# Performance work log

Measured on AMD Instinct MI355X. Metric: run time of the kernel, lower is better.

## Reference

```python
import jax, jax.numpy as jnp
import numpy as np

L, B, T, D, H, M = 2, 4, 1024, 256, 4, 1024
EPS = 1e-5  # hk.LayerNorm default


def setup_inputs() -> dict:
    key = jax.random.key(0)
    ks = jax.random.split(key, 12)
    s_in = (2.0 / D) ** 0.5       # VarianceScaling(2.0), fan_in = D
    s_o = (2.0 / (H * D)) ** 0.5  # fan_in = H*D for final projection
    s_m = (1.0 / M) ** 0.5
    g = lambda k, shape, s: jax.random.normal(k, shape, jnp.float32) * s
    return {
        "queries": g(ks[0], (B, T, D), 1.0),
        "Wq": g(ks[1], (L, D, H * D), s_in),
        "bq": jnp.zeros((L, H * D), jnp.float32),
        "Wk": g(ks[2], (L, D, H * D), s_in),
        "bk": jnp.zeros((L, H * D), jnp.float32),
        "Wv": g(ks[3], (L, D, H * D), s_in),
        "bv": jnp.zeros((L, H * D), jnp.float32),
        "Wo": g(ks[4], (L, H * D, D), s_o),
        "bo": jnp.zeros((L, D), jnp.float32),
        "ln1_s": jnp.ones((L, D), jnp.float32),
        "ln1_b": jnp.zeros((L, D), jnp.float32),
        "W1": g(ks[5], (L, D, M), s_in),
        "b1": jnp.zeros((L, M), jnp.float32),
        "W2": g(ks[6], (L, M, D), s_m),
        "b2": jnp.zeros((L, D), jnp.float32),
        "ln2_s": jnp.ones((L, D), jnp.float32),
        "ln2_b": jnp.zeros((L, D), jnp.float32),
    }


def _layernorm(x, s, o):
    m = jnp.mean(x, axis=-1, keepdims=True)
    v = jnp.var(x, axis=-1, keepdims=True)
    return (x - m) * jax.lax.rsqrt(v + EPS) * s + o


def _block(x, Wq, bq, Wk, bk, Wv, bv, Wo, bo, ln1_s, ln1_b, W1, b1, W2, b2, ln2_s, ln2_b):
    # Multi-head self-attention with per-head dim = D (key_size == qkv_size)
    q = (x @ Wq + bq).reshape(B, T, H, D)
    k = (x @ Wk + bk).reshape(B, T, H, D)
    v = (x @ Wv + bv).reshape(B, T, H, D)
    q = q / jnp.sqrt(jnp.float32(D))
    attn = jnp.einsum('bqhd,bkhd->bhqk', q, k)   # [B,H,T,T]
    attn = jax.nn.softmax(attn, axis=-1)
    o = jnp.einsum('bhqk,bkhd->bqhd', attn, v).reshape(B, T, H * D)
    o = o @ Wo + bo
    # post-norm residual 1
    x = _layernorm(o + x, ln1_s, ln1_b)
    # MLP: Linear(D->M) + ReLU + Linear(M->D)
    h = jax.nn.relu(x @ W1 + b1)
    m = h @ W2 + b2
    return _layernorm(m + x, ln2_s, ln2_b)


def reference(queries, Wq, bq, Wk, bk, Wv, bv, Wo, bo, ln1_s, ln1_b,
              W1, b1, W2, b2, ln2_s, ln2_b):
    x = queries
    for i in range(L):
        x = _block(x, Wq[i], bq[i], Wk[i], bk[i], Wv[i], bv[i], Wo[i], bo[i],
                   ln1_s[i], ln1_b[i], W1[i], b1[i], W2[i], b2[i],
                   ln2_s[i], ln2_b[i])
    return x
```

## Files before the change

### kernel.cpp

```cpp
#include <hip/hip_runtime.h>
#include <hip/hip_bf16.h>

#define CL 2
#define CB 4
#define CT 1024
#define CD 256
#define CH 4
#define CM 1024
#define CHD (CH * CD)
#define NROW (CB * CT)

typedef unsigned short ushort_t;
typedef __attribute__((ext_vector_type(8))) short short8v;
typedef __attribute__((ext_vector_type(4))) float float4v;

#define LOG2E 1.44269504088896f

__device__ __forceinline__ float bf2f(unsigned short u) {
    return __uint_as_float(((unsigned int)u) << 16);
}
__device__ __forceinline__ unsigned short f2bf(float f) {
    unsigned int x = __float_as_uint(f);
    return (unsigned short)((x + 0x7fffu + ((x >> 16) & 1u)) >> 16);
}

__global__ __launch_bounds__(256) void detect_kernel(
    const ushort_t* __restrict__ w, int n, int* __restrict__ flag)
{
    __shared__ int red[256];
    int c = 0;
    for (int i = threadIdx.x; i < n; i += 256) {
        float v = bf2f(w[i]);
        if (!(fabsf(v) <= 1e6f)) c++;
    }
    red[threadIdx.x] = c;
    __syncthreads();
    for (int s = 128; s > 0; s >>= 1) {
        if (threadIdx.x < s) red[threadIdx.x] += red[threadIdx.x + s];
        __syncthreads();
    }
    if (threadIdx.x == 0) flag[0] = (red[0] < 8) ? 1 : 0;
}

__global__ __launch_bounds__(256) void tconv_all(
    const void* __restrict__ Wq, const void* __restrict__ Wk,
    const void* __restrict__ Wv, const void* __restrict__ W1,
    ushort_t* __restrict__ wqkvT, ushort_t* __restrict__ w1T,
    const int* __restrict__ flagp)
{
    const int fbf = *flagp;
    const int z = blockIdx.z;
    const int which = z >> 1, l = z & 1;
    const void* in = (which == 0) ? Wq : (which == 1) ? Wk
                   : (which == 2) ? Wv : W1;
    ushort_t* out = (which < 3)
        ? wqkvT + (long)l * 3072 * 256 + (long)which * 1024 * 256
        : w1T + (long)l * 1024 * 256;
    const long zi = (long)l * 262144;

    __shared__ float tile[32][33];
    const int r0 = blockIdx.y * 32;
    const int c0 = blockIdx.x * 32;
    const int tx = threadIdx.x & 31;
    const int ty = threadIdx.x >> 5;
#pragma unroll
    for (int i = 0; i < 32; i += 8) {
        const long idx = zi + (long)(r0 + ty + i) * 1024 + c0 + tx;
        tile[ty + i][tx] = fbf ? bf2f(((const ushort_t*)in)[idx])
                               : ((const float*)in)[idx];
    }
    __syncthreads();
#pragma unroll
    for (int i = 0; i < 32; i += 8)
        out[(long)(c0 + ty + i) * 256 + r0 + tx] = f2bf(tile[tx][ty + i]);
}

__global__ __launch_bounds__(256) void tconv2(
    const void* __restrict__ Wo, const void* __restrict__ W2,
    ushort_t* __restrict__ wscr, long ioff, const int* __restrict__ flagp)
{
    const int fbf = *flagp;
    const int z = blockIdx.z;
    const void* in = z ? W2 : Wo;
    ushort_t* out = wscr + (long)z * 262144;

    __shared__ float tile[32][33];
    const int r0 = blockIdx.y * 32;
    const int c0 = blockIdx.x * 32;
    const int tx = threadIdx.x & 31;
    const int ty = threadIdx.x >> 5;
#pragma unroll
    for (int i = 0; i < 32; i += 8) {
        const long idx = ioff + (long)(r0 + ty + i) * 256 + c0 + tx;
        tile[ty + i][tx] = fbf ? bf2f(((const ushort_t*)in)[idx])
                               : ((const float*)in)[idx];
    }
    __syncthreads();
#pragma unroll
    for (int i = 0; i < 32; i += 8)
        out[(long)(c0 + ty + i) * 1024 + r0 + tx] = f2bf(tile[tx][ty + i]);
}

__global__ __launch_bounds__(256) void qkv_proj(
    const ushort_t* __restrict__ A, const ushort_t* __restrict__ B,
    const void* __restrict__ bq, const void* __restrict__ bk,
    const void* __restrict__ bv, ushort_t* __restrict__ qk,
    ushort_t* __restrict__ vT, long boff, const int* __restrict__ flagp)
{
    const long m0 = (long)blockIdx.y * 128;
    const long n0 = (long)blockIdx.x * 128;

    __shared__ __align__(16) ushort_t As[128 * 32];
    __shared__ __align__(16) ushort_t Bs[128 * 32];

    const int tid = threadIdx.x;
    const int wave = tid >> 6;
    const int lane = tid & 63;
    const int quad = lane >> 4;
    const int lrow = lane & 15;
    const int wm = (wave >> 1) * 64;
    const int wn = (wave & 1) * 64;

    float4v acc[4][4];
#pragma unroll
    for (int i = 0; i < 4; ++i)
#pragma unroll
        for (int j = 0; j < 4; ++j)
            acc[i][j] = (float4v){0.f, 0.f, 0.f, 0.f};

    for (int k0 = 0; k0 < 256; k0 += 32) {
        __syncthreads();
#pragma unroll
        for (int p = 0; p < 2; ++p) {
            const int c = p * 256 + tid;
            const int row = c >> 2;
            const int kk = (c & 3) << 3;
            *reinterpret_cast<short8v*>(&As[c << 3]) =
                *reinterpret_cast<const short8v*>(&A[(m0 + row) * 256 + k0 + kk]);
            *reinterpret_cast<short8v*>(&Bs[c << 3]) =
                *reinterpret_cast<const short8v*>(&B[(n0 + row) * 256 + k0 + kk]);
        }
        __syncthreads();

        short8v af[4], bfv[4];
#pragma unroll
        for (int i = 0; i < 4; ++i) {
            af[i]  = *reinterpret_cast<const short8v*>(&As[(wm + i * 16 + lrow) * 32 + quad * 8]);
            bfv[i] = *reinterpret_cast<const short8v*>(&Bs[(wn + i * 16 + lrow) * 32 + quad * 8]);
        }
#pragma unroll
        for (int mi = 0; mi < 4; ++mi)
#pragma unroll
            for (int ni = 0; ni < 4; ++ni)
                acc[mi][ni] = __builtin_amdgcn_mfma_f32_16x16x32_bf16(
                    af[mi], bfv[ni], acc[mi][ni], 0, 0, 0);
    }

    const int fbf = *flagp;
#pragma unroll
    for (int mi = 0; mi < 4; ++mi) {
#pragma unroll
        for (int ni = 0; ni < 4; ++ni) {
            const long col = n0 + wn + ni * 16 + lrow;
            const long row0 = m0 + wm + mi * 16 + quad * 4;
            const void* bp;
            long bn;
            if (col < 1024)      { bp = bq; bn = col; }
            else if (col < 2048) { bp = bk; bn = col - 1024; }
            else                 { bp = bv; bn = col - 2048; }
            const float bias = fbf ? bf2f(((const ushort_t*)bp)[boff + bn])
                                   : ((const float*)bp)[boff + bn];
            if (col < 2048) {
#pragma unroll
                for (int r = 0; r < 4; ++r)
                    qk[(row0 + r) * 2048 + col] = f2bf(acc[mi][ni][r] + bias);
            } else {
                const long d = col - 2048;
                const long addr = ((row0 >> 10) << 2) * 262144 + d * 1024 + (row0 & 1023);
                ushort4 u;
                u.x = f2bf(acc[mi][ni][0] + bias);
                u.y = f2bf(acc[mi][ni][1] + bias);
                u.z = f2bf(acc[mi][ni][2] + bias);
                u.w = f2bf(acc[mi][ni][3] + bias);
                *reinterpret_cast<ushort4*>(&vT[addr]) = u;
            }
        }
    }
}

template <int AMODE>
__global__ __launch_bounds__(256) void mgemm64s(
    const ushort_t* __restrict__ A, const ushort_t* __restrict__ Ap1,
    const float2* __restrict__ ml, const ushort_t* __restrict__ B,
    float* __restrict__ P, int K2, int lda, int ldb)
{
    const int z = blockIdx.z;
    const long m0 = (long)blockIdx.y * 64;
    const long n0 = (long)blockIdx.x * 64;
    const int k_beg = z * K2;

    __shared__ __align__(16) ushort_t As[64 * 32];
    __shared__ __align__(16) ushort_t Bs[64 * 32];

    const int tid = threadIdx.x;
    const int wave = tid >> 6;
    const int lane = tid & 63;
    const int quad = lane >> 4;
    const int lrow = lane & 15;
    const int wm = (wave >> 1) * 32;
    const int wn = (wave & 1) * 32;

    const int ar = tid >> 2;
    const int ak = (tid & 3) << 3;

    float4v acc[2][2];
#pragma unroll
    for (int i = 0; i < 2; ++i)
#pragma unroll
        for (int j = 0; j < 2; ++j)
            acc[i][j] = (float4v){0.f, 0.f, 0.f, 0.f};

    for (int k0 = k_beg; k0 < k_beg + K2; k0 += 32) {
        __syncthreads();
        if constexpr (AMODE == 0) {
            *reinterpret_cast<short8v*>(&As[tid << 3]) =
                *reinterpret_cast<const short8v*>(&A[(m0 + ar) * (long)lda + k0 + ak]);
        } else {
            const long m = m0 + ar;
            const int hh = (k0 + ak) >> 8;
            const int bh = ((int)(m >> 10) << 2) + hh;
            const int trow = (int)(m & 1023);
            const float2 v0 = ml[bh * 1024 + trow];
            const float2 v1 = ml[(16 + bh) * 1024 + trow];
            const float mm = fmaxf(v0.x, v1.x);
            const float a0 = exp2f(v0.x - mm);
            const float a1 = exp2f(v1.x - mm);
            const float inv = 1.0f / (v0.y * a0 + v1.y * a1);
            const ushort4 u0a = *reinterpret_cast<const ushort4*>(&A[m * 1024 + k0 + ak]);
            const ushort4 u0b = *reinterpret_cast<const ushort4*>(&A[m * 1024 + k0 + ak + 4]);
            const ushort4 u1a = *reinterpret_cast<const ushort4*>(&Ap1[m * 1024 + k0 + ak]);
            const ushort4 u1b = *reinterpret_cast<const ushort4*>(&Ap1[m * 1024 + k0 + ak + 4]);
            short8v t8;
            t8[0] = (short)f2bf((bf2f(u0a.x) * a0 + bf2f(u1a.x) * a1) * inv);
            t8[1] = (short)f2bf((bf2f(u0a.y) * a0 + bf2f(u1a.y) * a1) * inv);
            t8[2] = (short)f2bf((bf2f(u0a.z) * a0 + bf2f(u1a.z) * a1) * inv);
            t8[3] = (short)f2bf((bf2f(u0a.w) * a0 + bf2f(u1a.w) * a1) * inv);
            t8[4] = (short)f2bf((bf2f(u0b.x) * a0 + bf2f(u1b.x) * a1) * inv);
            t8[5] = (short)f2bf((bf2f(u0b.y) * a0 + bf2f(u1b.y) * a1) * inv);
            t8[6] = (short)f2bf((bf2f(u0b.z) * a0 + bf2f(u1b.z) * a1) * inv);
            t8[7] = (short)f2bf((bf2f(u0b.w) * a0 + bf2f(u1b.w) * a1) * inv);
            *reinterpret_cast<short8v*>(&As[tid << 3]) = t8;
        }
        *reinterpret_cast<short8v*>(&Bs[tid << 3]) =
            *reinterpret_cast<const short8v*>(&B[(n0 + ar) * (long)ldb + k0 + ak]);
        __syncthreads();

        short8v af[2], bfv[2];
#pragma unroll
        for (int i = 0; i < 2; ++i) {
            af[i]  = *reinterpret_cast<const short8v*>(&As[(wm + i * 16 + lrow) * 32 + quad * 8]);
            bfv[i] = *reinterpret_cast<const short8v*>(&Bs[(wn + i * 16 + lrow) * 32 + quad * 8]);
        }
#pragma unroll
        for (int mi = 0; mi < 2; ++mi)
#pragma unroll
            for (int ni = 0; ni < 2; ++ni)
                acc[mi][ni] = __builtin_amdgcn_mfma_f32_16x16x32_bf16(
                    af[mi], bfv[ni], acc[mi][ni], 0, 0, 0);
    }

    float* Pz = P + (long)z * NROW * CD;
#pragma unroll
    for (int mi = 0; mi < 2; ++mi)
#pragma unroll
        for (int ni = 0; ni < 2; ++ni) {
            const long col = n0 + wn + ni * 16 + lrow;
            const long row0 = m0 + wm + mi * 16 + quad * 4;
#pragma unroll
            for (int r = 0; r < 4; ++r)
                Pz[(row0 + r) * CD + col] = acc[mi][ni][r];
        }
}

template <int RELU>
__global__ __launch_bounds__(256) void mgemm64b(
    const ushort_t* __restrict__ A, const ushort_t* __restrict__ B,
    const void* __restrict__ bias, ushort_t* __restrict__ C,
    int K, int lda, int ldb, int ldc, long boff,
    const int* __restrict__ flagp)
{
    const long m0 = (long)blockIdx.y * 64;
    const long n0 = (long)blockIdx.x * 64;

    __shared__ __align__(16) ushort_t As[64 * 32];
    __shared__ __align__(16) ushort_t Bs[64 * 32];

    const int tid = threadIdx.x;
    const int wave = tid >> 6;
    const int lane = tid & 63;
    const int quad = lane >> 4;
    const int lrow = lane & 15;
    const int wm = (wave >> 1) * 32;
    const int wn = (wave & 1) * 32;

    const int ar = tid >> 2;
    const int ak = (tid & 3) << 3;

    float4v acc[2][2];
#pragma unroll
    for (int i = 0; i < 2; ++i)
#pragma unroll
        for (int j = 0; j < 2; ++j)
            acc[i][j] = (float4v){0.f, 0.f, 0.f, 0.f};

    for (int k0 = 0; k0 < K; k0 += 32) {
        __syncthreads();
        *reinterpret_cast<short8v*>(&As[tid << 3]) =
            *reinterpret_cast<const short8v*>(&A[(m0 + ar) * (long)lda + k0 + ak]);
        *reinterpret_cast<short8v*>(&Bs[tid << 3]) =
            *reinterpret_cast<const short8v*>(&B[(n0 + ar) * (long)ldb + k0 + ak]);
        __syncthreads();

        short8v af[2], bfv[2];
#pragma unroll
        for (int i = 0; i < 2; ++i) {
            af[i]  = *reinterpret_cast<const short8v*>(&As[(wm + i * 16 + lrow) * 32 + quad * 8]);
            bfv[i] = *reinterpret_cast<const short8v*>(&Bs[(wn + i * 16 + lrow) * 32 + quad * 8]);
        }
#pragma unroll
        for (int mi = 0; mi < 2; ++mi)
#pragma unroll
            for (int ni = 0; ni < 2; ++ni)
                acc[mi][ni] = __builtin_amdgcn_mfma_f32_16x16x32_bf16(
                    af[mi], bfv[ni], acc[mi][ni], 0, 0, 0);
    }

    const int fbf = *flagp;
#pragma unroll
    for (int mi = 0; mi < 2; ++mi)
#pragma unroll
        for (int ni = 0; ni < 2; ++ni) {
            const long col = n0 + wn + ni * 16 + lrow;
            const long row0 = m0 + wm + mi * 16 + quad * 4;
            const float bv = fbf ? bf2f(((const ushort_t*)bias)[boff + col])
                                 : ((const float*)bias)[boff + col];
#pragma unroll
            for (int r = 0; r < 4; ++r) {
                float v = acc[mi][ni][r] + bv;
                if (RELU) v = fmaxf(v, 0.f);
                C[(row0 + r) * (long)ldc + col] = f2bf(v);
            }
        }
}

__global__ __launch_bounds__(256) void flash_attn(
    const ushort_t* __restrict__ qk, const ushort_t* __restrict__ vT,
    ushort_t* __restrict__ op0, ushort_t* __restrict__ op1,
    float2* __restrict__ ml)
{
    const int bx = blockIdx.x;
    const int bh = bx & 15;
    const int qt = (bx >> 4) & 15;
    const int ck = bx >> 8;
    const int b = bh >> 2, h = bh & 3;

    __shared__ __align__(16) ushort_t Ks[32 * 264];
    __shared__ __align__(16) ushort_t Vs[256 * 40];
    __shared__ __align__(16) ushort_t Ps[4][16 * 40];

    const int tid = threadIdx.x;
    const int wave = tid >> 6;
    const int lane = tid & 63;
    const int quad = lane >> 4;
    const int lrow = lane & 15;

    const long qrow0 = (long)b * CT + qt * 64;
    const int qcol = h * 256;
    const int kcol = 1024 + h * 256;
    const long vbase = (long)bh * 256 * 1024;
    const float SC = 0.0625f * LOG2E;

    short8v qf[8];
#pragma unroll
    for (int kk = 0; kk < 8; ++kk)
        qf[kk] = *reinterpret_cast<const short8v*>(
            &qk[(qrow0 + wave * 16 + lrow) * 2048 + qcol + kk * 32 + quad * 8]);

    float mrun = -1e30f, lrun = 0.f;
    float4v oacc[16];
#pragma unroll
    for (int i = 0; i < 16; ++i) oacc[i] = (float4v){0.f, 0.f, 0.f, 0.f};

    const int t_beg = ck * 512;
    for (int t0 = t_beg; t0 < t_beg + 512; t0 += 32) {
        __syncthreads();
#pragma unroll
        for (int p = 0; p < 4; ++p) {
            const int c = p * 256 + tid;
            {
                const int r = c >> 5, col = (c & 31) * 8;
                *reinterpret_cast<short8v*>(&Ks[r * 264 + col]) =
                    *reinterpret_cast<const short8v*>(
                        &qk[((long)b * CT + t0 + r) * 2048 + kcol + col]);
            }
            {
                const int r = c >> 2, col = (c & 3) * 8;
                *reinterpret_cast<short8v*>(&Vs[r * 40 + col]) =
                    *reinterpret_cast<const short8v*>(
                        &vT[vbase + (long)r * 1024 + t0 + col]);
            }
        }
        __syncthreads();

        float4v sacc[2];
        sacc[0] = (float4v){0.f, 0.f, 0.f, 0.f};
        sacc[1] = (float4v){0.f, 0.f, 0.f, 0.f};
#pragma unroll
        for (int kk = 0; kk < 8; ++kk) {
#pragma unroll
            for (int ni = 0; ni < 2; ++ni) {
                short8v bk = *reinterpret_cast<const short8v*>(
                    &Ks[(ni * 16 + lrow) * 264 + kk * 32 + quad * 8]);
                sacc[ni] = __builtin_amdgcn_mfma_f32_16x16x32_bf16(
                    bk, qf[kk], sacc[ni], 0, 0, 0);
            }
        }
#pragma unroll
        for (int ni = 0; ni < 2; ++ni)
#pragma unroll
            for (int r = 0; r < 4; ++r)
                sacc[ni][r] *= SC;

        float mx = fmaxf(fmaxf(fmaxf(sacc[0][0], sacc[0][1]),
                               fmaxf(sacc[0][2], sacc[0][3])),
                         fmaxf(fmaxf(sacc[1][0], sacc[1][1]),
                               fmaxf(sacc[1][2], sacc[1][3])));
        mx = fmaxf(mx, __shfl_xor(mx, 16));
        mx = fmaxf(mx, __shfl_xor(mx, 32));
        const float mnew = fmaxf(mrun, mx);
        const float alpha = exp2f(mrun - mnew);
        mrun = mnew;

        float s = 0.f;
#pragma unroll
        for (int ni = 0; ni < 2; ++ni)
#pragma unroll
            for (int r = 0; r < 4; ++r) {
                const float pv = exp2f(sacc[ni][r] - mnew);
                s += pv;
                Ps[wave][lrow * 40 + ni * 16 + quad * 4 + r] = f2bf(pv);
            }
        s += __shfl_xor(s, 16);
        s += __shfl_xor(s, 32);
        lrun = lrun * alpha + s;

        if (__ballot(alpha < 1.0f) != 0ull) {
            float a4[4];
#pragma unroll
            for (int r = 0; r < 4; ++r)
                a4[r] = __shfl(alpha, quad * 4 + r);
#pragma unroll
            for (int ni = 0; ni < 16; ++ni)
#pragma unroll
                for (int r = 0; r < 4; ++r)
                    oacc[ni][r] *= a4[r];
        }

        {
            short8v ap = *reinterpret_cast<const short8v*>(
                &Ps[wave][lrow * 40 + quad * 8]);
#pragma unroll
            for (int ni = 0; ni < 16; ++ni) {
                short8v bv = *reinterpret_cast<const short8v*>(
                    &Vs[(ni * 16 + lrow) * 40 + quad * 8]);
                oacc[ni] = __builtin_amdgcn_mfma_f32_16x16x32_bf16(
                    ap, bv, oacc[ni], 0, 0, 0);
            }
        }
    }

    if (quad == 0)
        ml[((ck << 4) + bh) * 1024 + qt * 64 + wave * 16 + lrow] =
            make_float2(mrun, lrun);

    ushort_t* op = ck ? op1 : op0;
#pragma unroll
    for (int ni = 0; ni < 16; ++ni)
#pragma unroll
        for (int r = 0; r < 4; ++r)
            op[(qrow0 + wave * 16 + quad * 4 + r) * 1024 + (h << 8) + ni * 16 + lrow]
                = f2bf(oacc[ni][r]);
}

template <int FINAL>
__global__ __launch_bounds__(256) void ln_p(
    const float* __restrict__ p, const void* __restrict__ gb, long gboff,
    const ushort_t* __restrict__ res, const void* __restrict__ sc,
    const void* __restrict__ bi, void* __restrict__ out, long loff,
    const int* __restrict__ flagp)
{
    const int fbf = *flagp;
    const long row = (long)blockIdx.x * CD;
    const int t = threadIdx.x;
    const float gbv = fbf ? bf2f(((const ushort_t*)gb)[gboff + t])
                          : ((const float*)gb)[gboff + t];
    const float x = p[row + t] + p[(long)NROW * CD + row + t] + gbv + bf2f(res[row + t]);

    __shared__ float r1[256];
    __shared__ float r2[256];
    r1[t] = x;
    r2[t] = x * x;
    __syncthreads();
    for (int s = 128; s > 0; s >>= 1) {
        if (t < s) { r1[t] += r1[t + s]; r2[t] += r2[t + s]; }
        __syncthreads();
    }
    const float mean = r1[0] * (1.0f / CD);
    const float var = r2[0] * (1.0f / CD) - mean * mean;
    const float rstd = rsqrtf(var + 1e-5f);
    const float s_v = fbf ? bf2f(((const ushort_t*)sc)[loff + t]) : ((const float*)sc)[loff + t];
    const float b_v = fbf ? bf2f(((const ushort_t*)bi)[loff + t]) : ((const float*)bi)[loff + t];
    const float y = (x - mean) * rstd * s_v + b_v;
    if constexpr (FINAL) {
        if (fbf) ((ushort_t*)out)[row + t] = f2bf(y);
        else     ((float*)out)[row + t] = y;
    } else {
        ((ushort_t*)out)[row + t] = f2bf(y);
    }
}

__global__ __launch_bounds__(256) void in_convert(
    const void* __restrict__ in, ushort_t* __restrict__ x,
    const int* __restrict__ flagp)
{
    const int fbf = *flagp;
    const long i = ((long)blockIdx.x * 256 + threadIdx.x) << 2;
    if (fbf) {
        *reinterpret_cast<ushort4*>(x + i) =
            *reinterpret_cast<const ushort4*>((const ushort_t*)in + i);
    } else {
        float4 f = *reinterpret_cast<const float4*>((const float*)in + i);
        ushort4 u;
        u.x = f2bf(f.x); u.y = f2bf(f.y); u.z = f2bf(f.z); u.w = f2bf(f.w);
        *reinterpret_cast<ushort4*>(x + i) = u;
    }
}

extern "C" void kernel_launch(void* const* d_in, const int* in_sizes, int n_in,
                              void* d_out, int out_size, void* d_ws, size_t ws_size,
                              hipStream_t stream)
{
    const void* queries = d_in[0];
    const void* Wq = d_in[1];  const void* bq = d_in[2];
    const void* Wk = d_in[3];  const void* bk = d_in[4];
    const void* Wv = d_in[5];  const void* bv = d_in[6];
    const void* Wo = d_in[7];  const void* bo = d_in[8];
    const void* ln1s = d_in[9];  const void* ln1b = d_in[10];
    const void* W1 = d_in[11]; const void* b1 = d_in[12];
    const void* W2 = d_in[13]; const void* b2 = d_in[14];
    const void* ln2s = d_in[15]; const void* ln2b = d_in[16];

    char* p = (char*)d_ws;
    int* flagp = (int*)p;             p += 256;
    ushort_t* wqkvT = (ushort_t*)p;   p += (long)CL * 3072 * 256 * 2;
    ushort_t* w1T   = (ushort_t*)p;   p += (long)CL * 1024 * 256 * 2;
    ushort_t* wscr  = (ushort_t*)p;   p += (long)2 * 256 * 1024 * 2;
    ushort_t* xa    = (ushort_t*)p;   p += (long)NROW * CD * 2;
    ushort_t* qk    = (ushort_t*)p;   p += (long)NROW * 2048 * 2;
    ushort_t* vT    = (ushort_t*)p;   p += (long)16 * 256 * 1024 * 2;
    ushort_t* op0   = (ushort_t*)p;   p += (long)NROW * 1024 * 2;
    ushort_t* op1   = (ushort_t*)p;   p += (long)NROW * 1024 * 2;
    float2*   ml    = (float2*)p;     p += (long)2 * 16 * 1024 * 8;
    ushort_t* h     = vT;
    float*    pgem  = (float*)qk;

    detect_kernel<<<1, 256, 0, stream>>>((const ushort_t*)Wq, 2048, flagp);

    tconv_all<<<dim3(32, 8, 8), 256, 0, stream>>>(
        Wq, Wk, Wv, W1, wqkvT, w1T, flagp);

    in_convert<<<(NROW * CD) / 1024, 256, 0, stream>>>(queries, xa, flagp);

    for (int l = 0; l < CL; ++l) {
        qkv_proj<<<dim3(24, 32, 1), 256, 0, stream>>>(
            xa, wqkvT + (long)l * 3072 * 256, bq, bk, bv, qk, vT,
            (long)l * 1024, flagp);
        tconv2<<<dim3(8, 32, 2), 256, 0, stream>>>(
            Wo, W2, wscr, (long)l * 1024 * 256, flagp);
        flash_attn<<<512, 256, 0, stream>>>(qk, vT, op0, op1, ml);
        mgemm64s<1><<<dim3(4, 64, 2), 256, 0, stream>>>(
            op0, op1, ml, wscr, pgem, 512, 1024, 1024);
        ln_p<0><<<NROW, 256, 0, stream>>>(pgem, bo, (long)l * 256, xa,
                                          ln1s, ln1b, xa, (long)l * 256, flagp);
        mgemm64b<1><<<dim3(16, 64, 1), 256, 0, stream>>>(
            xa, w1T + (long)l * 1024 * 256, b1, h,
            256, 256, 256, 1024, (long)l * 1024, flagp);
        mgemm64s<0><<<dim3(4, 64, 2), 256, 0, stream>>>(
            h, nullptr, nullptr, wscr + 262144, pgem, 512, 1024, 1024);
        if (l == CL - 1)
            ln_p<1><<<NROW, 256, 0, stream>>>(pgem, b2, (long)l * 256, xa,
                                              ln2s, ln2b, d_out, (long)l * 256, flagp);
        else
            ln_p<0><<<NROW, 256, 0, stream>>>(pgem, b2, (long)l * 256, xa,
                                              ln2s, ln2b, xa, (long)l * 256, flagp);
    }
}
```

Baseline: 316.9 us.

## Fuse output and MLP-down GEMMs with LayerNorm, pad LDS, lazily rescale attention

```diff
diff --git a/kernel.cpp b/kernel.cpp
--- a/kernel.cpp
+++ b/kernel.cpp
@@ -110,8 +110,8 @@
     const long m0 = (long)blockIdx.y * 128;
     const long n0 = (long)blockIdx.x * 128;
 
-    __shared__ __align__(16) ushort_t As[128 * 32];
-    __shared__ __align__(16) ushort_t Bs[128 * 32];
+    __shared__ __align__(16) ushort_t As[128 * 40];
+    __shared__ __align__(16) ushort_t Bs[128 * 40];
 
     const int tid = threadIdx.x;
     const int wave = tid >> 6;
@@ -135,9 +135,9 @@
             const int c = p * 256 + tid;
             const int row = c >> 2;
             const int kk = (c & 3) << 3;
-            *reinterpret_cast<short8v*>(&As[c << 3]) =
+            *reinterpret_cast<short8v*>(&As[row * 40 + kk]) =
                 *reinterpret_cast<const short8v*>(&A[(m0 + row) * 256 + k0 + kk]);
-            *reinterpret_cast<short8v*>(&Bs[c << 3]) =
+            *reinterpret_cast<short8v*>(&Bs[row * 40 + kk]) =
                 *reinterpret_cast<const short8v*>(&B[(n0 + row) * 256 + k0 + kk]);
         }
         __syncthreads();
@@ -145,8 +145,8 @@
         short8v af[4], bfv[4];
 #pragma unroll
         for (int i = 0; i < 4; ++i) {
-            af[i]  = *reinterpret_cast<const short8v*>(&As[(wm + i * 16 + lrow) * 32 + quad * 8]);
-            bfv[i] = *reinterpret_cast<const short8v*>(&Bs[(wn + i * 16 + lrow) * 32 + quad * 8]);
+            af[i]  = *reinterpret_cast<const short8v*>(&As[(wm + i * 16 + lrow) * 40 + quad * 8]);
+            bfv[i] = *reinterpret_cast<const short8v*>(&Bs[(wn + i * 16 + lrow) * 40 + quad * 8]);
         }
 #pragma unroll
         for (int mi = 0; mi < 4; ++mi)
@@ -188,19 +188,18 @@
     }
 }
 
-template <int AMODE>
-__global__ __launch_bounds__(256) void mgemm64s(
-    const ushort_t* __restrict__ A, const ushort_t* __restrict__ Ap1,
-    const float2* __restrict__ ml, const ushort_t* __restrict__ B,
-    float* __restrict__ P, int K2, int lda, int ldb)
-{
-    const int z = blockIdx.z;
+template <int RELU>
+__global__ __launch_bounds__(256) void mgemm64b(
+    const ushort_t* __restrict__ A, const ushort_t* __restrict__ B,
+    const void* __restrict__ bias, ushort_t* __restrict__ C,
+    int K, int lda, int ldb, int ldc, long boff,
+    const int* __restrict__ flagp)
+{
     const long m0 = (long)blockIdx.y * 64;
     const long n0 = (long)blockIdx.x * 64;
-    const int k_beg = z * K2;
-
-    __shared__ __align__(16) ushort_t As[64 * 32];
-    __shared__ __align__(16) ushort_t Bs[64 * 32];
+
+    __shared__ __align__(16) ushort_t As[64 * 40];
+    __shared__ __align__(16) ushort_t Bs[64 * 40];
 
     const int tid = threadIdx.x;
     const int wave = tid >> 6;
@@ -220,14 +219,74 @@
         for (int j = 0; j < 2; ++j)
             acc[i][j] = (float4v){0.f, 0.f, 0.f, 0.f};
 
-    for (int k0 = k_beg; k0 < k_beg + K2; k0 += 32) {
-        __syncthreads();
-        if constexpr (AMODE == 0) {
-            *reinterpret_cast<short8v*>(&As[tid << 3]) =
-                *reinterpret_cast<const short8v*>(&A[(m0 + ar) * (long)lda + k0 + ak]);
-        } else {
-            const long m = m0 + ar;
-            const int hh = (k0 + ak) >> 8;
+    for (int k0 = 0; k0 < K; k0 += 32) {
+        __syncthreads();
+        *reinterpret_cast<short8v*>(&As[ar * 40 + ak]) =
+            *reinterpret_cast<const short8v*>(&A[(m0 + ar) * (long)lda + k0 + ak]);
+        *reinterpret_cast<short8v*>(&Bs[ar * 40 + ak]) =
+            *reinterpret_cast<const short8v*>(&B[(n0 + ar) * (long)ldb + k0 + ak]);
+        __syncthreads();
+
+        short8v af[2], bfv[2];
+#pragma unroll
+        for (int i = 0; i < 2; ++i) {
+            af[i]  = *reinterpret_cast<const short8v*>(&As[(wm + i * 16 + lrow) * 40 + quad * 8]);
+            bfv[i] = *reinterpret_cast<const short8v*>(&Bs[(wn + i * 16 + lrow) * 40 + quad * 8]);
+        }
+#pragma unroll
+        for (int mi = 0; mi < 2; ++mi)
+#pragma unroll
+            for (int ni = 0; ni < 2; ++ni)
+                acc[mi][ni] = __builtin_amdgcn_mfma_f32_16x16x32_bf16(
+                    af[mi], bfv[ni], acc[mi][ni], 0, 0, 0);
+    }
+
+    const int fbf = *flagp;
+#pragma unroll
+    for (int mi = 0; mi < 2; ++mi)
+#pragma unroll
+        for (int ni = 0; ni < 2; ++ni) {
+            const long col = n0 + wn + ni * 16 + lrow;
+            const long row0 = m0 + wm + mi * 16 + quad * 4;
+            const float bv = fbf ? bf2f(((const ushort_t*)bias)[boff + col])
+                                 : ((const float*)bias)[boff + col];
+#pragma unroll
+            for (int r = 0; r < 4; ++r) {
+                float v = acc[mi][ni][r] + bv;
+                if (RELU) v = fmaxf(v, 0.f);
+                C[(row0 + r) * (long)ldc + col] = f2bf(v);
+            }
+        }
+}
+
+template <int AMODE, int FINAL>
+__global__ __launch_bounds__(256) void gemm_ln(
+    const ushort_t* __restrict__ A, const ushort_t* __restrict__ Ap1,
+    const float2* __restrict__ ml, const ushort_t* __restrict__ B,
+    const void* __restrict__ gb, long goff,
+    const ushort_t* __restrict__ res, const void* __restrict__ sc,
+    const void* __restrict__ bi, void* __restrict__ out, long loff,
+    const int* __restrict__ flagp)
+{
+    const long m0 = (long)blockIdx.x * 16;
+
+    __shared__ __align__(16) ushort_t As[16 * 40];
+    __shared__ __align__(16) ushort_t Bs[256 * 40];
+    __shared__ float mlc[16][4][2];
+    __shared__ float red1[4][16];
+    __shared__ float red2[4][16];
+    __shared__ float stat[2][16];
+
+    const int tid = threadIdx.x;
+    const int wave = tid >> 6;
+    const int lane = tid & 63;
+    const int quad = lane >> 4;
+    const int lrow = lane & 15;
+
+    if constexpr (AMODE == 1) {
+        if (tid < 64) {
+            const int r = tid >> 2, hh = tid & 3;
+            const long m = m0 + r;
             const int bh = ((int)(m >> 10) << 2) + hh;
             const int trow = (int)(m & 1023);
             const float2 v0 = ml[bh * 1024 + trow];
@@ -236,121 +295,117 @@
             const float a0 = exp2f(v0.x - mm);
             const float a1 = exp2f(v1.x - mm);
             const float inv = 1.0f / (v0.y * a0 + v1.y * a1);
-            const ushort4 u0a = *reinterpret_cast<const ushort4*>(&A[m * 1024 + k0 + ak]);
-            const ushort4 u0b = *reinterpret_cast<const ushort4*>(&A[m * 1024 + k0 + ak + 4]);
-            const ushort4 u1a = *reinterpret_cast<const ushort4*>(&Ap1[m * 1024 + k0 + ak]);
-            const ushort4 u1b = *reinterpret_cast<const ushort4*>(&Ap1[m * 1024 + k0 + ak + 4]);
-            short8v t8;
-            t8[0] = (short)f2bf((bf2f(u0a.x) * a0 + bf2f(u1a.x) * a1) * inv);
-            t8[1] = (short)f2bf((bf2f(u0a.y) * a0 + bf2f(u1a.y) * a1) * inv);
-            t8[2] = (short)f2bf((bf2f(u0a.z) * a0 + bf2f(u1a.z) * a1) * inv);
-            t8[3] = (short)f2bf((bf2f(u0a.w) * a0 + bf2f(u1a.w) * a1) * inv);
-            t8[4] = (short)f2bf((bf2f(u0b.x) * a0 + bf2f(u1b.x) * a1) * inv);
-            t8[5] = (short)f2bf((bf2f(u0b.y) * a0 + bf2f(u1b.y) * a1) * inv);
-            t8[6] = (short)f2bf((bf2f(u0b.z) * a0 + bf2f(u1b.z) * a1) * inv);
-            t8[7] = (short)f2bf((bf2f(u0b.w) * a0 + bf2f(u1b.w) * a1) * inv);
-            *reinterpret_cast<short8v*>(&As[tid << 3]) = t8;
-        }
-        *reinterpret_cast<short8v*>(&Bs[tid << 3]) =
-            *reinterpret_cast<const short8v*>(&B[(n0 + ar) * (long)ldb + k0 + ak]);
-        __syncthreads();
-
-        short8v af[2], bfv[2];
-#pragma unroll
-        for (int i = 0; i < 2; ++i) {
-            af[i]  = *reinterpret_cast<const short8v*>(&As[(wm + i * 16 + lrow) * 32 + quad * 8]);
-            bfv[i] = *reinterpret_cast<const short8v*>(&Bs[(wn + i * 16 + lrow) * 32 + quad * 8]);
-        }
-#pragma unroll
-        for (int mi = 0; mi < 2; ++mi)
-#pragma unroll
-            for (int ni = 0; ni < 2; ++ni)
-                acc[mi][ni] = __builtin_amdgcn_mfma_f32_16x16x32_bf16(
-                    af[mi], bfv[ni], acc[mi][ni], 0, 0, 0);
-    }
-
-    float* Pz = P + (long)z * NROW * CD;
-#pragma unroll
-    for (int mi = 0; mi < 2; ++mi)
-#pragma unroll
-        for (int ni = 0; ni < 2; ++ni) {
-            const long col = n0 + wn + ni * 16 + lrow;
-            const long row0 = m0 + wm + mi * 16 + quad * 4;
-#pragma unroll
-            for (int r = 0; r < 4; ++r)
-                Pz[(row0 + r) * CD + col] = acc[mi][ni][r];
-        }
-}
-
-template <int RELU>
-__global__ __launch_bounds__(256) void mgemm64b(
-    const ushort_t* __restrict__ A, const ushort_t* __restrict__ B,
-    const void* __restrict__ bias, ushort_t* __restrict__ C,
-    int K, int lda, int ldb, int ldc, long boff,
-    const int* __restrict__ flagp)
-{
-    const long m0 = (long)blockIdx.y * 64;
-    const long n0 = (long)blockIdx.x * 64;
-
-    __shared__ __align__(16) ushort_t As[64 * 32];
-    __shared__ __align__(16) ushort_t Bs[64 * 32];
-
-    const int tid = threadIdx.x;
-    const int wave = tid >> 6;
-    const int lane = tid & 63;
-    const int quad = lane >> 4;
-    const int lrow = lane & 15;
-    const int wm = (wave >> 1) * 32;
-    const int wn = (wave & 1) * 32;
-
-    const int ar = tid >> 2;
-    const int ak = (tid & 3) << 3;
-
-    float4v acc[2][2];
-#pragma unroll
-    for (int i = 0; i < 2; ++i)
-#pragma unroll
-        for (int j = 0; j < 2; ++j)
-            acc[i][j] = (float4v){0.f, 0.f, 0.f, 0.f};
-
-    for (int k0 = 0; k0 < K; k0 += 32) {
-        __syncthreads();
-        *reinterpret_cast<short8v*>(&As[tid << 3]) =
-            *reinterpret_cast<const short8v*>(&A[(m0 + ar) * (long)lda + k0 + ak]);
-        *reinterpret_cast<short8v*>(&Bs[tid << 3]) =
-            *reinterpret_cast<const short8v*>(&B[(n0 + ar) * (long)ldb + k0 + ak]);
-        __syncthreads();
-
-        short8v af[2], bfv[2];
-#pragma unroll
-        for (int i = 0; i < 2; ++i) {
-            af[i]  = *reinterpret_cast<const short8v*>(&As[(wm + i * 16 + lrow) * 32 + quad * 8]);
-            bfv[i] = *reinterpret_cast<const short8v*>(&Bs[(wn + i * 16 + lrow) * 32 + quad * 8]);
-        }
-#pragma unroll
-        for (int mi = 0; mi < 2; ++mi)
-#pragma unroll
-            for (int ni = 0; ni < 2; ++ni)
-                acc[mi][ni] = __builtin_amdgcn_mfma_f32_16x16x32_bf16(
-                    af[mi], bfv[ni], acc[mi][ni], 0, 0, 0);
+            mlc[r][hh][0] = a0 * inv;
+            mlc[r][hh][1] = a1 * inv;
+        }
+    }
+
+    float4v acc[4];
+#pragma unroll
+    for (int i = 0; i < 4; ++i) acc[i] = (float4v){0.f, 0.f, 0.f, 0.f};
+
+    for (int k0 = 0; k0 < 1024; k0 += 32) {
+        __syncthreads();
+        {
+            const int row = tid >> 4;
+            const int c2 = (tid & 15) << 1;
+            const long ga = (m0 + row) * 1024 + k0 + c2;
+            if constexpr (AMODE == 0) {
+                *reinterpret_cast<ushort2*>(&As[row * 40 + c2]) =
+                    *reinterpret_cast<const ushort2*>(&A[ga]);
+            } else {
+                const int hh = k0 >> 8;
+                const float s0 = mlc[row][hh][0];
+                const float s1 = mlc[row][hh][1];
+                const ushort2 p0 = *reinterpret_cast<const ushort2*>(&A[ga]);
+                const ushort2 p1 = *reinterpret_cast<const ushort2*>(&Ap1[ga]);
+                ushort2 o;
+                o.x = f2bf(bf2f(p0.x) * s0 + bf2f(p1.x) * s1);
+                o.y = f2bf(bf2f(p0.y) * s0 + bf2f(p1.y) * s1);
+                *reinterpret_cast<ushort2*>(&As[row * 40 + c2]) = o;
+            }
+        }
+#pragma unroll
+        for (int p = 0; p < 4; ++p) {
+            const int c = p * 256 + tid;
+            const int n = c >> 2, kc = (c & 3) << 3;
+            *reinterpret_cast<short8v*>(&Bs[n * 40 + kc]) =
+                *reinterpret_cast<const short8v*>(&B[(long)n * 1024 + k0 + kc]);
+        }
+        __syncthreads();
+
+        short8v af = *reinterpret_cast<const short8v*>(&As[lrow * 40 + quad * 8]);
+#pragma unroll
+        for (int ni = 0; ni < 4; ++ni) {
+            short8v bfv = *reinterpret_cast<const short8v*>(
+                &Bs[(wave * 64 + ni * 16 + lrow) * 40 + quad * 8]);
+            acc[ni] = __builtin_amdgcn_mfma_f32_16x16x32_bf16(af, bfv, acc[ni], 0, 0, 0);
+        }
     }
 
     const int fbf = *flagp;
-#pragma unroll
-    for (int mi = 0; mi < 2; ++mi)
-#pragma unroll
-        for (int ni = 0; ni < 2; ++ni) {
-            const long col = n0 + wn + ni * 16 + lrow;
-            const long row0 = m0 + wm + mi * 16 + quad * 4;
-            const float bv = fbf ? bf2f(((const ushort_t*)bias)[boff + col])
-                                 : ((const float*)bias)[boff + col];
-#pragma unroll
-            for (int r = 0; r < 4; ++r) {
-                float v = acc[mi][ni][r] + bv;
-                if (RELU) v = fmaxf(v, 0.f);
-                C[(row0 + r) * (long)ldc + col] = f2bf(v);
-            }
-        }
+    float x[4][4];
+    float s1[4] = {0.f, 0.f, 0.f, 0.f}, s2[4] = {0.f, 0.f, 0.f, 0.f};
+#pragma unroll
+    for (int ni = 0; ni < 4; ++ni) {
+        const int col = wave * 64 + ni * 16 + lrow;
+        const float gbv = fbf ? bf2f(((const ushort_t*)gb)[goff + col])
+                              : ((const float*)gb)[goff + col];
+#pragma unroll
+        for (int r = 0; r < 4; ++r) {
+            const long row = m0 + quad * 4 + r;
+            const float v = acc[ni][r] + gbv + bf2f(res[row * 256 + col]);
+            x[ni][r] = v;
+            s1[r] += v;
+            s2[r] += v * v;
+        }
+    }
+#pragma unroll
+    for (int r = 0; r < 4; ++r) {
+#pragma unroll
+        for (int sh = 1; sh < 16; sh <<= 1) {
+            s1[r] += __shfl_xor(s1[r], sh);
+            s2[r] += __shfl_xor(s2[r], sh);
+        }
+    }
+    if (lrow == 0) {
+#pragma unroll
+        for (int r = 0; r < 4; ++r) {
+            red1[wave][quad * 4 + r] = s1[r];
+            red2[wave][quad * 4 + r] = s2[r];
+        }
+    }
+    __syncthreads();
+    if (tid < 16) {
+        const float t1 = red1[0][tid] + red1[1][tid] + red1[2][tid] + red1[3][tid];
+        const float t2 = red2[0][tid] + red2[1][tid] + red2[2][tid] + red2[3][tid];
+        const float mean = t1 * (1.0f / 256.0f);
+        const float var = t2 * (1.0f / 256.0f) - mean * mean;
+        stat[0][tid] = mean;
+        stat[1][tid] = rsqrtf(var + 1e-5f);
+    }
+    __syncthreads();
+
+#pragma unroll
+    for (int ni = 0; ni < 4; ++ni) {
+        const int col = wave * 64 + ni * 16 + lrow;
+        const float scv = fbf ? bf2f(((const ushort_t*)sc)[loff + col])
+                              : ((const float*)sc)[loff + col];
+        const float biv = fbf ? bf2f(((const ushort_t*)bi)[loff + col])
+                              : ((const float*)bi)[loff + col];
+#pragma unroll
+        for (int r = 0; r < 4; ++r) {
+            const int rr = quad * 4 + r;
+            const float y = (x[ni][r] - stat[0][rr]) * stat[1][rr] * scv + biv;
+            const long oidx = (m0 + rr) * 256 + col;
+            if constexpr (FINAL) {
+                if (fbf) ((ushort_t*)out)[oidx] = f2bf(y);
+                else     ((float*)out)[oidx] = y;
+            } else {
+                ((ushort_t*)out)[oidx] = f2bf(y);
+            }
+        }
+    }
 }
 
 __global__ __launch_bounds__(256) void flash_attn(
@@ -437,34 +492,39 @@
                                fmaxf(sacc[1][2], sacc[1][3])));
         mx = fmaxf(mx, __shfl_xor(mx, 16));
         mx = fmaxf(mx, __shfl_xor(mx, 32));
-        const float mnew = fmaxf(mrun, mx);
-        const float alpha = exp2f(mrun - mnew);
-        mrun = mnew;
+
+        if (__ballot(mx > mrun + 1.0f) != 0ull) {
+            const float mnew = fmaxf(mrun, mx);
+            const float alpha = exp2f(mrun - mnew);
+            mrun = mnew;
+            lrun *= alpha;
+            float a4[4];
+#pragma unroll
+            for (int r = 0; r < 4; ++r)
+                a4[r] = __shfl(alpha, quad * 4 + r);
+#pragma unroll
+            for (int ni = 0; ni < 16; ++ni)
+#pragma unroll
+                for (int r = 0; r < 4; ++r)
+                    oacc[ni][r] *= a4[r];
+        }
 
         float s = 0.f;
 #pragma unroll
-        for (int ni = 0; ni < 2; ++ni)
+        for (int ni = 0; ni < 2; ++ni) {
+            ushort4 pu;
 #pragma unroll
             for (int r = 0; r < 4; ++r) {
-                const float pv = exp2f(sacc[ni][r] - mnew);
+                const float pv = exp2f(sacc[ni][r] - mrun);
                 s += pv;
-                Ps[wave][lrow * 40 + ni * 16 + quad * 4 + r] = f2bf(pv);
-            }
+                (&pu.x)[r] = f2bf(pv);
+            }
+            *reinterpret_cast<ushort4*>(
+                &Ps[wave][lrow * 40 + ni * 16 + quad * 4]) = pu;
+        }
         s += __shfl_xor(s, 16);
         s += __shfl_xor(s, 32);
-        lrun = lrun * alpha + s;
-
-        if (__ballot(alpha < 1.0f) != 0ull) {
-            float a4[4];
-#pragma unroll
-            for (int r = 0; r < 4; ++r)
-                a4[r] = __shfl(alpha, quad * 4 + r);
-#pragma unroll
-            for (int ni = 0; ni < 16; ++ni)
-#pragma unroll
-                for (int r = 0; r < 4; ++r)
-                    oacc[ni][r] *= a4[r];
-        }
+        lrun += s;
 
         {
             short8v ap = *reinterpret_cast<const short8v*>(
@@ -490,43 +550,6 @@
         for (int r = 0; r < 4; ++r)
             op[(qrow0 + wave * 16 + quad * 4 + r) * 1024 + (h << 8) + ni * 16 + lrow]
                 = f2bf(oacc[ni][r]);
-}
-
-template <int FINAL>
-__global__ __launch_bounds__(256) void ln_p(
-    const float* __restrict__ p, const void* __restrict__ gb, long gboff,
-    const ushort_t* __restrict__ res, const void* __restrict__ sc,
-    const void* __restrict__ bi, void* __restrict__ out, long loff,
-    const int* __restrict__ flagp)
-{
-    const int fbf = *flagp;
-    const long row = (long)blockIdx.x * CD;
-    const int t = threadIdx.x;
-    const float gbv = fbf ? bf2f(((const ushort_t*)gb)[gboff + t])
-                          : ((const float*)gb)[gboff + t];
-    const float x = p[row + t] + p[(long)NROW * CD + row + t] + gbv + bf2f(res[row + t]);
-
-    __shared__ float r1[256];
-    __shared__ float r2[256];
-    r1[t] = x;
-    r2[t] = x * x;
-    __syncthreads();
-    for (int s = 128; s > 0; s >>= 1) {
-        if (t < s) { r1[t] += r1[t + s]; r2[t] += r2[t + s]; }
-        __syncthreads();
-    }
-    const float mean = r1[0] * (1.0f / CD);
-    const float var = r2[0] * (1.0f / CD) - mean * mean;
-    const float rstd = rsqrtf(var + 1e-5f);
-    const float s_v = fbf ? bf2f(((const ushort_t*)sc)[loff + t]) : ((const float*)sc)[loff + t];
-    const float b_v = fbf ? bf2f(((const ushort_t*)bi)[loff + t]) : ((const float*)bi)[loff + t];
-    const float y = (x - mean) * rstd * s_v + b_v;
-    if constexpr (FINAL) {
-        if (fbf) ((ushort_t*)out)[row + t] = f2bf(y);
-        else     ((float*)out)[row + t] = y;
-    } else {
-        ((ushort_t*)out)[row + t] = f2bf(y);
-    }
 }
 
 __global__ __launch_bounds__(256) void in_convert(
@@ -572,13 +595,10 @@
     ushort_t* op1   = (ushort_t*)p;   p += (long)NROW * 1024 * 2;
     float2*   ml    = (float2*)p;     p += (long)2 * 16 * 1024 * 8;
     ushort_t* h     = vT;
-    float*    pgem  = (float*)qk;
 
     detect_kernel<<<1, 256, 0, stream>>>((const ushort_t*)Wq, 2048, flagp);
-
     tconv_all<<<dim3(32, 8, 8), 256, 0, stream>>>(
         Wq, Wk, Wv, W1, wqkvT, w1T, flagp);
-
     in_convert<<<(NROW * CD) / 1024, 256, 0, stream>>>(queries, xa, flagp);
 
     for (int l = 0; l < CL; ++l) {
@@ -588,20 +608,19 @@
         tconv2<<<dim3(8, 32, 2), 256, 0, stream>>>(
             Wo, W2, wscr, (long)l * 1024 * 256, flagp);
         flash_attn<<<512, 256, 0, stream>>>(qk, vT, op0, op1, ml);
-        mgemm64s<1><<<dim3(4, 64, 2), 256, 0, stream>>>(
-            op0, op1, ml, wscr, pgem, 512, 1024, 1024);
-        ln_p<0><<<NROW, 256, 0, stream>>>(pgem, bo, (long)l * 256, xa,
-                                          ln1s, ln1b, xa, (long)l * 256, flagp);
+        gemm_ln<1, 0><<<256, 256, 0, stream>>>(
+            op0, op1, ml, wscr, bo, (long)l * 256, xa, ln1s, ln1b, xa,
+            (long)l * 256, flagp);
         mgemm64b<1><<<dim3(16, 64, 1), 256, 0, stream>>>(
             xa, w1T + (long)l * 1024 * 256, b1, h,
             256, 256, 256, 1024, (long)l * 1024, flagp);
-        mgemm64s<0><<<dim3(4, 64, 2), 256, 0, stream>>>(
-            h, nullptr, nullptr, wscr + 262144, pgem, 512, 1024, 1024);
         if (l == CL - 1)
-            ln_p<1><<<NROW, 256, 0, stream>>>(pgem, b2, (long)l * 256, xa,
-                                              ln2s, ln2b, d_out, (long)l * 256, flagp);
+            gemm_ln<0, 1><<<256, 256, 0, stream>>>(
+                h, nullptr, nullptr, wscr + 262144, b2, (long)l * 256, xa,
+                ln2s, ln2b, d_out, (long)l * 256, flagp);
         else
-            ln_p<0><<<NROW, 256, 0, stream>>>(pgem, b2, (long)l * 256, xa,
-                                              ln2s, ln2b, xa, (long)l * 256, flagp);
-    }
-}
+            gemm_ln<0, 0><<<256, 256, 0, stream>>>(
+                h, nullptr, nullptr, wscr + 262144, b2, (long)l * 256, xa,
+                ln2s, ln2b, xa, (long)l * 256, flagp);
+    }
+}
```

New measurement: 339.1 us. 1.07x slower.
